# Kernel tuning notes

Hardware: AMD Instinct MI355X
Metric: run time of the kernel (lower is better)

The kernel has to match this reference:

```python
import jax, jax.numpy as jnp
import numpy as np
from jax import lax

B, C_IN, T = 32, 80, 1000
C = 512          # encoder_embedding_dim
H = C // 2       # LSTM hidden per direction
K = 5            # kernel size
P_ZONEOUT = 0.1
BN_EPS = 1e-5


def setup_inputs() -> dict:
    key = jax.random.key(0)
    ks = jax.random.split(key, 32)
    d = {"x": jax.random.normal(ks[0], (B, C_IN, T), jnp.float32)}
    in_chs = [C_IN, C, C]
    i = 1
    for l in range(3):
        cin = in_chs[l]
        d[f"cw{l}"] = jax.random.normal(ks[i], (C, cin, K), jnp.float32) * (1.0 / np.sqrt(cin * K)); i += 1
        d[f"cb{l}"] = jnp.zeros((C,), jnp.float32)
        d[f"bg{l}"] = jnp.ones((C,), jnp.float32)
        d[f"bb{l}"] = jnp.zeros((C,), jnp.float32)
        d[f"bm{l}"] = jax.random.normal(ks[i], (C,), jnp.float32) * 0.1; i += 1
        d[f"bv{l}"] = jax.random.uniform(ks[i], (C,), jnp.float32, 0.5, 1.5); i += 1
    for tag in ("f", "b"):
        d[f"wih_{tag}"] = jax.random.normal(ks[i], (4 * H, C), jnp.float32) * (1.0 / np.sqrt(C)); i += 1
        d[f"whh_{tag}"] = jax.random.normal(ks[i], (4 * H, H), jnp.float32) * (1.0 / np.sqrt(H)); i += 1
        d[f"bih_{tag}"] = jnp.zeros((4 * H,), jnp.float32)
        d[f"bhh_{tag}"] = jnp.zeros((4 * H,), jnp.float32)
    return d


def _lstm_cell(xt, h, c, wih, whh, bih, bhh):
    g = xt @ wih.T + bih + h @ whh.T + bhh          # [B, 4H]
    i, f, gg, o = jnp.split(g, 4, axis=-1)
    c2 = jax.nn.sigmoid(f) * c + jax.nn.sigmoid(i) * jnp.tanh(gg)
    h2 = jax.nn.sigmoid(o) * jnp.tanh(c2)
    return h2, c2


def _zoneout(old, new, p):
    return p * old + (1.0 - p) * new


def _encoder(x, conv_params, lstm_params):
    # conv + BN(eval) + ReLU stack; dropout is identity in eval mode
    for (cw, cb, bg, bb, bm, bv) in conv_params:
        x = lax.conv_general_dilated(x, cw, (1,), [((K - 1) // 2, (K - 1) // 2)],
                                     dimension_numbers=("NCH", "OIH", "NCH"))
        x = x + cb[None, :, None]
        x = (x - bm[None, :, None]) * (bg / jnp.sqrt(bv + BN_EPS))[None, :, None] + bb[None, :, None]
        x = jax.nn.relu(x)
    x = x.transpose(0, 2, 1)                         # [B, T, C]
    (wih_f, whh_f, bih_f, bhh_f, wih_b, whh_b, bih_b, bhh_b) = lstm_params

    xs_f = x.transpose(1, 0, 2)                      # [T, B, C] forward order
    xs_b = xs_f[::-1]                                # backward order

    def step(carry, inp):
        hf, cf, hb, cb_ = carry
        xf, xb = inp
        hf2, cf2 = _lstm_cell(xf, hf, cf, wih_f, whh_f, bih_f, bhh_f)
        hb2, cb2 = _lstm_cell(xb, hb, cb_, wih_b, whh_b, bih_b, bhh_b)
        hf = _zoneout(hf, hf2, P_ZONEOUT); cf = _zoneout(cf, cf2, P_ZONEOUT)
        hb = _zoneout(hb, hb2, P_ZONEOUT); cb_ = _zoneout(cb_, cb2, P_ZONEOUT)
        return (hf, cf, hb, cb_), (hf, hb)

    z = jnp.zeros((x.shape[0], H), x.dtype)
    _, (out_f, out_b) = lax.scan(step, (z, z, z, z), (xs_f, xs_b))
    out = jnp.concatenate([out_f, out_b[::-1]], axis=-1)  # [T, B, 2H]
    return out.transpose(1, 0, 2)                         # [B, T, 2H]


def reference(x, cw0, cb0, bg0, bb0, bm0, bv0,
              cw1, cb1, bg1, bb1, bm1, bv1,
              cw2, cb2, bg2, bb2, bm2, bv2,
              wih_f, whh_f, bih_f, bhh_f,
              wih_b, whh_b, bih_b, bhh_b):
    conv_params = [(cw0, cb0, bg0, bb0, bm0, bv0),
                   (cw1, cb1, bg1, bb1, bm1, bv1),
                   (cw2, cb2, bg2, bb2, bm2, bv2)]
    lstm_params = (wih_f, whh_f, bih_f, bhh_f, wih_b, whh_b, bih_b, bhh_b)
    return _encoder(x, conv_params, lstm_params)
```

## Files before the change

### kernel.cpp

```cpp
#include <hip/hip_runtime.h>


#define T_LEN 1000
#define NBATCH 32
#define CCH 512
#define HDIM 256
#define GDIM 1024
#define TC 100

typedef _Float16 h16;
typedef _Float16 h16x2 __attribute__((ext_vector_type(2)));
typedef _Float16 f16x8 __attribute__((ext_vector_type(8)));
typedef float    f32x4 __attribute__((ext_vector_type(4)));

__device__ __forceinline__ float fixup(float v, float alt){
    union { float f; unsigned u; } c; c.f = v;
    return ((c.u & 0x7f800000u) == 0x7f800000u) ? alt : v;
}
__device__ __forceinline__ float clamp_s(float v, float lo, float hi){
    return fminf(fmaxf(v, lo), hi);
}
__device__ __forceinline__ float sigm(float x){
    const float xc = clamp_s(x, -30.f, 30.f);
    return 1.0f / (1.0f + __expf(-xc));
}
__device__ __forceinline__ float tanh_safe(float x){
    const float ax = fminf(fabsf(x), 30.0f);
    const float t  = __expf(-2.0f * ax);
    const float r  = (1.0f - t) / (1.0f + t);
    return copysignf(r, x);
}
__device__ __forceinline__ int dot4i8(int a, int b, int c){
#if defined(__has_builtin) && __has_builtin(__builtin_amdgcn_sdot4)
    return __builtin_amdgcn_sdot4(a, b, c, false);
#else
    int r = c;
    #pragma unroll
    for (int k = 0; k < 4; ++k) {
        const int av = (a << (24 - 8*k)) >> 24;
        const int bv = (b << (24 - 8*k)) >> 24;
        r += av * bv;
    }
    return r;
#endif
}

__global__ __launch_bounds__(256)
void pack_convw_kernel(const float* __restrict__ cw, h16* __restrict__ Wp, int cin)
{
    const int n = blockIdx.x*256 + threadIdx.x;
    if (n >= 5*512*cin) return;
    const int k   = n / (512*cin);
    const int rem = n - k*512*cin;
    const int co  = rem / cin;
    const int ci  = rem - co*cin;
    Wp[n] = (h16)cw[((size_t)co*cin + ci)*5 + k];
}

__global__ __launch_bounds__(256)
void pack_wih_kernel(const float* __restrict__ wf, const float* __restrict__ wb, h16* __restrict__ Wg)
{
    const int n = blockIdx.x*256 + threadIdx.x;
    const float* src = (n < 1024*512) ? wf : wb;
    Wg[n] = (h16)src[n & (1024*512 - 1)];
}

__global__ __launch_bounds__(256)
void whh_scale_kernel(const float* __restrict__ whh_f, const float* __restrict__ whh_b,
                      float* __restrict__ scl)
{
    const int n = blockIdx.x*256 + threadIdx.x;
    if (n >= 2048) return;
    const float* whh = (n >= 1024) ? whh_b : whh_f;
    const int row = n & 1023;
    float m = 0.f;
    for (int k = 0; k < HDIM; ++k) m = fmaxf(m, fabsf(whh[(size_t)row*HDIM + k]));
    scl[n] = fmaxf(m, 1e-8f) / 16129.0f;
}

__global__ __launch_bounds__(256)
void whh_prep_kernel(const float* __restrict__ whh_f, const float* __restrict__ whh_b,
                     const float* __restrict__ scl, unsigned* __restrict__ W8)
{
    const int n = blockIdx.x * 256 + threadIdx.x;
    if (n >= 2*16*1024*4) return;
    const int dir   = n >> 16;
    const int rem   = n & 65535;
    const int chunk = rem >> 12;
    const int idx   = rem & 4095;
    const int t     = idx >> 2;
    const int e     = idx & 3;
    const float* whh = dir ? whh_b : whh_f;
    const int half = (t >> 6) & 1;
    const int qq   = t >> 7;
    const int l    = t & 63;
    const int rA   = qq*128 + 2*l;
    int row, g;
    if (chunk < 8)        { row = rA + 1; g = chunk; }
    else if (chunk < 11)  { row = rA;     g = chunk - 3; }
    else                  { row = rA;     g = chunk - 11; }
    const float inv = 1.0f / (scl[dir*1024 + row] * 127.0f);
    const int k0 = 128*half + 16*g + 4*e;
    unsigned u = 0;
    #pragma unroll
    for (int j = 0; j < 4; ++j) {
        const float w = whh[(size_t)row*HDIM + k0 + j];
        int qv = (int)rintf(w * inv);
        qv = qv > 127 ? 127 : (qv < -127 ? -127 : qv);
        u |= ((unsigned)(qv & 0xFF)) << (8*j);
    }
    W8[n] = u;
}

__global__ __launch_bounds__(256)
void x0_transpose_kernel(const float* __restrict__ x, h16* __restrict__ Xt0)
{
    const int b = blockIdx.y;
    const int t = blockIdx.x*256 + threadIdx.x;
    if (t >= T_LEN) return;
    h16 v[80];
    #pragma unroll
    for (int c = 0; c < 80; ++c) v[c] = (h16)x[((size_t)b*80 + c)*T_LEN + t];
    #pragma unroll
    for (int g = 0; g < 10; ++g)
        *(f16x8*)(Xt0 + ((size_t)b*T_LEN + t)*80 + g*8) = *(const f16x8*)(v + g*8);
}

template<int CIN>
__global__ __attribute__((amdgpu_flat_work_group_size(512,512), amdgpu_waves_per_eu(2,4)))
void conv_mfma_kernel(const h16* __restrict__ Xt, const h16* __restrict__ Wp,
                      h16* __restrict__ outp,
                      const float* __restrict__ cb, const float* __restrict__ bg,
                      const float* __restrict__ bb, const float* __restrict__ bm,
                      const float* __restrict__ bv)
{
    const int t0   = blockIdx.x * 256;
    const int co0  = blockIdx.y * 128;
    const int b    = blockIdx.z;
    const int tid  = threadIdx.x;
    const int lane = tid & 63;
    const int w    = tid >> 6;
    const int wm   = w >> 1;
    const int wn   = w & 1;
    const int lr   = lane & 15;
    const int lg   = lane >> 4;

    __shared__ __align__(16) h16 Xs[260*40];
    __shared__ __align__(16) h16 Ws[5*128*40];

    f32x4 acc[4][4];
    #pragma unroll
    for (int m = 0; m < 4; ++m)
        #pragma unroll
        for (int n = 0; n < 4; ++n)
            #pragma unroll
            for (int r = 0; r < 4; ++r) acc[m][n][r] = 0.f;

    constexpr int KSTEPS = (CIN + 31) >> 5;
    for (int cs = 0; cs < KSTEPS; ++cs) {
        const int c0 = cs << 5;
        for (int id = tid; id < 260*4; id += 512) {
            const int row = id >> 2, g = id & 3;
            const int t = t0 + row - 2;
            f16x8 v;
            #pragma unroll
            for (int j = 0; j < 8; ++j) v[j] = (h16)0.f;
            if (t >= 0 && t < T_LEN) {
                const int c = c0 + g*8;
                if (c + 8 <= CIN) {
                    v = *(const f16x8*)(Xt + ((size_t)b*T_LEN + t)*CIN + c);
                } else if (c < CIN) {
                    #pragma unroll
                    for (int j = 0; j < 8; ++j) if (c + j < CIN) v[j] = Xt[((size_t)b*T_LEN + t)*CIN + c + j];
                }
            }
            *(f16x8*)(Xs + row*40 + g*8) = v;
        }
        for (int id = tid; id < 5*128*4; id += 512) {
            const int k  = id >> 9;
            const int co = (id >> 2) & 127;
            const int g  = id & 3;
            const int c  = c0 + g*8;
            f16x8 v;
            #pragma unroll
            for (int j = 0; j < 8; ++j) v[j] = (h16)0.f;
            if (c + 8 <= CIN) {
                v = *(const f16x8*)(Wp + ((size_t)k*512 + co0 + co)*CIN + c);
            } else if (c < CIN) {
                #pragma unroll
                for (int j = 0; j < 8; ++j) if (c + j < CIN) v[j] = Wp[((size_t)k*512 + co0 + co)*CIN + c + j];
            }
            *(f16x8*)(Ws + (k*128 + co)*40 + g*8) = v;
        }
        __syncthreads();

        #pragma unroll
        for (int k = 0; k < 5; ++k) {
            f16x8 bfr[4];
            #pragma unroll
            for (int nf = 0; nf < 4; ++nf)
                bfr[nf] = *(const f16x8*)(Ws + (k*128 + wn*64 + nf*16 + lr)*40 + lg*8);
            #pragma unroll
            for (int m = 0; m < 4; ++m) {
                const f16x8 a = *(const f16x8*)(Xs + (wm*64 + m*16 + lr + k)*40 + lg*8);
                #pragma unroll
                for (int nf = 0; nf < 4; ++nf)
                    acc[m][nf] = __builtin_amdgcn_mfma_f32_16x16x32_f16(a, bfr[nf], acc[m][nf], 0, 0, 0);
            }
        }
        __syncthreads();
    }

    #pragma unroll
    for (int nf = 0; nf < 4; ++nf) {
        const int co = co0 + wn*64 + nf*16 + lr;
        const float s  = bg[co] * rsqrtf(fmaxf(bv[co] + 1e-5f, 1e-8f));
        const float sh = (cb[co] - bm[co]) * s + bb[co];
        #pragma unroll
        for (int m = 0; m < 4; ++m) {
            #pragma unroll
            for (int r = 0; r < 4; ++r) {
                const int t = t0 + wm*64 + m*16 + lg*4 + r;
                if (t < T_LEN) {
                    const float y = fixup(clamp_s(fmaxf(acc[m][nf][r]*s + sh, 0.f), 0.f, 60000.f), 0.f);
                    outp[((size_t)b*T_LEN + t)*CCH + co] = (h16)y;
                }
            }
        }
    }
}

__global__ __attribute__((amdgpu_flat_work_group_size(256,256), amdgpu_waves_per_eu(4,4)))
void gates_mfma_kernel(const h16* __restrict__ Xt,
                       const h16* __restrict__ Wg,
                       const float* __restrict__ bih_f, const float* __restrict__ bhh_f,
                       const float* __restrict__ bih_b, const float* __restrict__ bhh_b,
                       h16* __restrict__ G, int t0f, int t0b)
{
    const int tt   = blockIdx.x;
    const int r0   = blockIdx.y * 128;
    const int b    = blockIdx.z & 31;
    const int dir  = blockIdx.z >> 5;
    const int t0c  = dir ? t0b : t0f;
    const int tid  = threadIdx.x;
    const int lane = tid & 63;
    const int w    = tid >> 6;
    const int lr   = lane & 15;
    const int lg   = lane >> 4;
    const float* bi = dir ? bih_b : bih_f;
    const float* bh = dir ? bhh_b : bhh_f;
    const h16* Wd = Wg + (size_t)dir*1024*512;

    __shared__ __align__(16) h16 Xs[64*40];
    __shared__ __align__(16) h16 Ws[128*40];

    f32x4 acc[4][2];
    #pragma unroll
    for (int m = 0; m < 4; ++m)
        #pragma unroll
        for (int n = 0; n < 2; ++n)
            #pragma unroll
            for (int r = 0; r < 4; ++r) acc[m][n][r] = 0.f;

    for (int cs = 0; cs < 16; ++cs) {
        const int c0 = cs << 5;
        for (int id = tid; id < 64*4; id += 256) {
            const int row = id >> 2, g = id & 3;
            int t = t0c + tt*64 + row; if (t >= T_LEN) t = T_LEN - 1;
            *(f16x8*)(Xs + row*40 + g*8) = *(const f16x8*)(Xt + ((size_t)b*T_LEN + t)*CCH + c0 + g*8);
        }
        for (int id = tid; id < 128*4; id += 256) {
            const int row = id >> 2, g = id & 3;
            *(f16x8*)(Ws + row*40 + g*8) = *(const f16x8*)(Wd + (size_t)(r0 + row)*CCH + c0 + g*8);
        }
        __syncthreads();

        const f16x8 b0 = *(const f16x8*)(Ws + (w*32 +      lr)*40 + lg*8);
        const f16x8 b1 = *(const f16x8*)(Ws + (w*32 + 16 + lr)*40 + lg*8);
        #pragma unroll
        for (int m = 0; m < 4; ++m) {
            const f16x8 a = *(const f16x8*)(Xs + (m*16 + lr)*40 + lg*8);
            acc[m][0] = __builtin_amdgcn_mfma_f32_16x16x32_f16(a, b0, acc[m][0], 0, 0, 0);
            acc[m][1] = __builtin_amdgcn_mfma_f32_16x16x32_f16(a, b1, acc[m][1], 0, 0, 0);
        }
        __syncthreads();
    }

    #pragma unroll
    for (int nf = 0; nf < 2; ++nf) {
        const int row = r0 + w*32 + nf*16 + lr;
        const float bias = bi[row] + bh[row];
        #pragma unroll
        for (int m = 0; m < 4; ++m) {
            #pragma unroll
            for (int r = 0; r < 4; ++r) {
                const int tl = tt*64 + m*16 + lg*4 + r;
                if (tl < TC)
                    G[(((size_t)dir*TC + tl)*NBATCH + b)*GDIM + row]
                        = (h16)fixup(clamp_s(acc[m][nf][r] + bias, -60000.f, 60000.f), 0.f);
            }
        }
    }
}

__global__ __attribute__((amdgpu_flat_work_group_size(1024, 1024), amdgpu_waves_per_eu(4, 4)))
void lstm_chunk_kernel(const h16* __restrict__ G,
                       const unsigned* __restrict__ W8,
                       const float* __restrict__ scl,
                       float* __restrict__ state,
                       float* __restrict__ out,
                       int t0f, int t0b, int first)
{
    const int tid  = threadIdx.x;
    const int lane = tid & 63;
    const int half = (tid >> 6) & 1;
    const int q    = tid >> 7;
    const int dir  = blockIdx.x >> 5;
    const int b    = blockIdx.x & 31;
    const int t0   = dir ? t0b : t0f;
    float* st = state + ((size_t)(dir*NBATCH + b))*2*HDIM;
    const uint4* Wg8 = (const uint4*)W8 + (size_t)dir*16384;

    __shared__ __align__(16) uint4 lw8[5*1024];
    __shared__ __align__(4)  unsigned char hq8[256];
    __shared__ float pbuf[2*GDIM];

    uint4 rb[8];
    #pragma unroll
    for (int g = 0; g < 8; ++g) rb[g] = Wg8[g*1024 + tid];
    uint4 ra0 = Wg8[8*1024 + tid];
    uint4 ra1 = Wg8[9*1024 + tid];
    uint4 ra2 = Wg8[10*1024 + tid];

    #pragma unroll
    for (int s = 0; s < 5; ++s)
        lw8[s*1024 + tid] = Wg8[(11 + s)*1024 + tid];

    const int rA = q*128 + 2*lane;
    const float sclA = scl[dir*1024 + rA];
    const float sclB = scl[dir*1024 + rA + 1];

    float hst = 0.0f, cst = 0.0f;
    if (tid < HDIM) {
        if (!first) { hst = st[tid]; cst = st[HDIM + tid]; }
        const int qh = (int)rintf(clamp_s(hst, -1.f, 1.f) * 127.f);
        hq8[tid] = (unsigned char)(qh & 0xFF);
    }
    __syncthreads();

    float2* pbuf2 = (float2*)pbuf;
    float prev_h = 0.0f;
    int   prev_t = -1;

    for (int i = 0; i < TC; ++i) {
        const int sl = dir ? (TC - 1 - i) : i;
        const int t  = t0 + sl;
        const h16* gp = G + (((size_t)dir*TC + sl)*NBATCH + b)*GDIM;

        const unsigned wv = ((const unsigned*)hq8)[(half << 5) | (lane & 31)];

        float g0 = 0.f, g1 = 0.f, g2 = 0.f, g3 = 0.f;
        if (tid < HDIM) {
            if (prev_t >= 0)
                out[((size_t)b*T_LEN + prev_t)*(2*HDIM) + dir*HDIM + tid] = prev_h;
            g0 = (float)gp[tid];
            g1 = (float)gp[HDIM + tid];
            g2 = (float)gp[2*HDIM + tid];
            g3 = (float)gp[3*HDIM + tid];
        }

        int accA = 0, accB = 0;
        #pragma unroll
        for (int g = 0; g < 8; ++g) {
            const int s0 = __builtin_amdgcn_readlane((int)wv, 4*g + 0);
            const int s1 = __builtin_amdgcn_readlane((int)wv, 4*g + 1);
            const int s2 = __builtin_amdgcn_readlane((int)wv, 4*g + 2);
            const int s3 = __builtin_amdgcn_readlane((int)wv, 4*g + 3);
            const uint4 wA = (g < 5) ? lw8[g*1024 + tid]
                                     : (g == 5 ? ra0 : (g == 6 ? ra1 : ra2));
            const uint4 wB = rb[g];
            accA = dot4i8(s0, (int)wA.x, accA);
            accA = dot4i8(s1, (int)wA.y, accA);
            accA = dot4i8(s2, (int)wA.z, accA);
            accA = dot4i8(s3, (int)wA.w, accA);
            accB = dot4i8(s0, (int)wB.x, accB);
            accB = dot4i8(s1, (int)wB.y, accB);
            accB = dot4i8(s2, (int)wB.z, accB);
            accB = dot4i8(s3, (int)wB.w, accB);
        }

        pbuf2[(half << 9) | (q << 6) | lane] = make_float2((float)accA * sclA, (float)accB * sclB);
        __syncthreads();

        if (tid < HDIM) {
            const float gi = g0 + pbuf[tid]            + pbuf[GDIM + tid];
            const float gf = g1 + pbuf[HDIM + tid]     + pbuf[GDIM + HDIM + tid];
            const float gg = g2 + pbuf[2*HDIM + tid]   + pbuf[GDIM + 2*HDIM + tid];
            const float go = g3 + pbuf[3*HDIM + tid]   + pbuf[GDIM + 3*HDIM + tid];
            const float c2 = sigm(gf)*cst + sigm(gi)*tanh_safe(gg);
            const float h2 = sigm(go)*tanh_safe(c2);
            hst = 0.1f*hst + 0.9f*h2;
            cst = 0.1f*cst + 0.9f*c2;
            prev_h = fixup(hst, 50.0f);
            prev_t = t;
            const int qh = (int)rintf(clamp_s(hst, -1.f, 1.f) * 127.f);
            hq8[tid] = (unsigned char)(qh & 0xFF);
        }
        __syncthreads();
    }

    if (tid < HDIM) {
        if (prev_t >= 0)
            out[((size_t)b*T_LEN + prev_t)*(2*HDIM) + dir*HDIM + tid] = prev_h;
        st[tid] = hst; st[HDIM + tid] = cst;
    }
}

extern "C" void kernel_launch(void* const* d_in, const int* in_sizes, int n_in,
                              void* d_out, int out_size, void* d_ws, size_t ws_size,
                              hipStream_t stream)
{
    (void)in_sizes; (void)n_in; (void)out_size;
    if (ws_size < 49152000) return;

    const float* x     = (const float*)d_in[0];
    const float* cw0   = (const float*)d_in[1];
    const float* cb0   = (const float*)d_in[2];
    const float* bg0   = (const float*)d_in[3];
    const float* bb0   = (const float*)d_in[4];
    const float* bm0   = (const float*)d_in[5];
    const float* bv0   = (const float*)d_in[6];
    const float* cw1   = (const float*)d_in[7];
    const float* cb1   = (const float*)d_in[8];
    const float* bg1   = (const float*)d_in[9];
    const float* bb1   = (const float*)d_in[10];
    const float* bm1   = (const float*)d_in[11];
    const float* bv1   = (const float*)d_in[12];
    const float* cw2   = (const float*)d_in[13];
    const float* cb2   = (const float*)d_in[14];
    const float* bg2   = (const float*)d_in[15];
    const float* bb2   = (const float*)d_in[16];
    const float* bm2   = (const float*)d_in[17];
    const float* bv2   = (const float*)d_in[18];
    const float* wih_f = (const float*)d_in[19];
    const float* whh_f = (const float*)d_in[20];
    const float* bih_f = (const float*)d_in[21];
    const float* bhh_f = (const float*)d_in[22];
    const float* wih_b = (const float*)d_in[23];
    const float* whh_b = (const float*)d_in[24];
    const float* bih_b = (const float*)d_in[25];
    const float* bhh_b = (const float*)d_in[26];

    char* ws = (char*)d_ws;
    char* od = (char*)d_out;
    h16*      A   = (h16*)(ws);
    h16*      G   = (h16*)(ws + 32768000);
    float*    st  = (float*)(ws + 45875200);
    unsigned* W8  = (unsigned*)(ws + 46006272);
    float*    scl = (float*)(ws + 46530560);
    h16*      Wg  = (h16*)(ws + 47054848);
    h16*      Bd  = (h16*)(od);
    h16*      Wp0 = (h16*)(od + 36000000);
    h16*      Wp1 = (h16*)(od + 36409600);
    h16*      Wp2 = (h16*)(od + 41652480);
    h16*      Xt0 = (h16*)(od + 46895360);
    float*    out = (float*)d_out;

    pack_convw_kernel<<<dim3((5*512*80  + 255)/256), 256, 0, stream>>>(cw0, Wp0, 80);
    pack_convw_kernel<<<dim3((5*512*512 + 255)/256), 256, 0, stream>>>(cw1, Wp1, 512);
    pack_convw_kernel<<<dim3((5*512*512 + 255)/256), 256, 0, stream>>>(cw2, Wp2, 512);
    pack_wih_kernel<<<dim3(2*1024*512/256), 256, 0, stream>>>(wih_f, wih_b, Wg);
    whh_scale_kernel<<<dim3(8), 256, 0, stream>>>(whh_f, whh_b, scl);
    whh_prep_kernel<<<dim3(512), 256, 0, stream>>>(whh_f, whh_b, scl, W8);
    x0_transpose_kernel<<<dim3(4, 32), 256, 0, stream>>>(x, Xt0);

    const dim3 cgrid(4, 4, 32);
    conv_mfma_kernel<80> <<<cgrid, 512, 0, stream>>>(Xt0, Wp0, A,  cb0, bg0, bb0, bm0, bv0);
    conv_mfma_kernel<512><<<cgrid, 512, 0, stream>>>(A,   Wp1, Bd, cb1, bg1, bb1, bm1, bv1);
    conv_mfma_kernel<512><<<cgrid, 512, 0, stream>>>(Bd,  Wp2, A,  cb2, bg2, bb2, bm2, bv2);

    for (int c = 0; c < T_LEN / TC; ++c) {
        const int t0f = c * TC;
        const int t0b = (T_LEN - TC) - c * TC;
        gates_mfma_kernel<<<dim3(2, 8, 64), 256, 0, stream>>>(A, Wg, bih_f, bhh_f, bih_b, bhh_b, G, t0f, t0b);
        lstm_chunk_kernel<<<dim3(64), 1024, 0, stream>>>(G, W8, scl, st, out, t0f, t0b, c == 0);
    }
}
```

Baseline: 1.665 ms.

## Restructure LSTM recurrence to one thread per hidden unit with register weights

The recurrent LSTM kernel now runs 256 threads per block instead of 1024. Each thread owns one hidden unit and holds all four gate rows of int8 W_hh in 64 uint4 registers. The weight prep layout is rewritten to match, and a double-buffered hidden-state array leaves one barrier per step instead of two, removing the shared partial-sum buffer and cross-thread reduction. In exchange each thread does four times the dot-product work serially with very high register pressure (1 wave per EU), which may cause spills or lengthen the per-step critical path.

```diff
diff --git a/kernel.cpp b/kernel.cpp
--- a/kernel.cpp
+++ b/kernel.cpp
@@ -83,33 +83,28 @@
                      const float* __restrict__ scl, unsigned* __restrict__ W8)
 {
     const int n = blockIdx.x * 256 + threadIdx.x;
-    if (n >= 2*16*1024*4) return;
-    const int dir   = n >> 16;
-    const int rem   = n & 65535;
-    const int chunk = rem >> 12;
-    const int idx   = rem & 4095;
-    const int t     = idx >> 2;
-    const int e     = idx & 3;
+    if (n >= 2*64*1024) return;
+    const int dir  = n >> 16;
+    const int rem  = n & 65535;
+    const int slot = rem >> 10;
+    const int idx  = rem & 1023;
+    const int u    = idx >> 2;
+    const int e    = idx & 3;
     const float* whh = dir ? whh_b : whh_f;
-    const int half = (t >> 6) & 1;
-    const int qq   = t >> 7;
-    const int l    = t & 63;
-    const int rA   = qq*128 + 2*l;
-    int row, g;
-    if (chunk < 8)        { row = rA + 1; g = chunk; }
-    else if (chunk < 11)  { row = rA;     g = chunk - 3; }
-    else                  { row = rA;     g = chunk - 11; }
+    const int rg  = slot >> 4;
+    const int jj  = slot & 15;
+    const int row = rg*256 + u;
     const float inv = 1.0f / (scl[dir*1024 + row] * 127.0f);
-    const int k0 = 128*half + 16*g + 4*e;
-    unsigned u = 0;
+    const int k0 = 16*jj + 4*e;
+    unsigned uv = 0;
     #pragma unroll
     for (int j = 0; j < 4; ++j) {
         const float w = whh[(size_t)row*HDIM + k0 + j];
         int qv = (int)rintf(w * inv);
         qv = qv > 127 ? 127 : (qv < -127 ? -127 : qv);
-        u |= ((unsigned)(qv & 0xFF)) << (8*j);
-    }
-    W8[n] = u;
+        uv |= ((unsigned)(qv & 0xFF)) << (8*j);
+    }
+    W8[n] = uv;
 }
 
 __global__ __launch_bounds__(256)
@@ -303,7 +298,7 @@
     }
 }
 
-__global__ __attribute__((amdgpu_flat_work_group_size(1024, 1024), amdgpu_waves_per_eu(4, 4)))
+__global__ __attribute__((amdgpu_flat_work_group_size(256, 256), amdgpu_waves_per_eu(1, 1)))
 void lstm_chunk_kernel(const h16* __restrict__ G,
                        const unsigned* __restrict__ W8,
                        const float* __restrict__ scl,
@@ -311,109 +306,81 @@
                        float* __restrict__ out,
                        int t0f, int t0b, int first)
 {
-    const int tid  = threadIdx.x;
-    const int lane = tid & 63;
-    const int half = (tid >> 6) & 1;
-    const int q    = tid >> 7;
+    const int u    = threadIdx.x;
+    const int lane = u & 63;
     const int dir  = blockIdx.x >> 5;
     const int b    = blockIdx.x & 31;
     const int t0   = dir ? t0b : t0f;
     float* st = state + ((size_t)(dir*NBATCH + b))*2*HDIM;
-    const uint4* Wg8 = (const uint4*)W8 + (size_t)dir*16384;
-
-    __shared__ __align__(16) uint4 lw8[5*1024];
-    __shared__ __align__(4)  unsigned char hq8[256];
-    __shared__ float pbuf[2*GDIM];
-
-    uint4 rb[8];
-    #pragma unroll
-    for (int g = 0; g < 8; ++g) rb[g] = Wg8[g*1024 + tid];
-    uint4 ra0 = Wg8[8*1024 + tid];
-    uint4 ra1 = Wg8[9*1024 + tid];
-    uint4 ra2 = Wg8[10*1024 + tid];
-
-    #pragma unroll
-    for (int s = 0; s < 5; ++s)
-        lw8[s*1024 + tid] = Wg8[(11 + s)*1024 + tid];
-
-    const int rA = q*128 + 2*lane;
-    const float sclA = scl[dir*1024 + rA];
-    const float sclB = scl[dir*1024 + rA + 1];
+    const uint4* Wv = (const uint4*)W8 + (size_t)dir*16384;
+
+    __shared__ __align__(4) unsigned char hq8[2][256];
+
+    uint4 wr[64];
+    #pragma unroll
+    for (int s = 0; s < 64; ++s) wr[s] = Wv[s*256 + u];
+
+    const float s0 = scl[dir*1024 +       u];
+    const float s1 = scl[dir*1024 + 256 + u];
+    const float s2 = scl[dir*1024 + 512 + u];
+    const float s3 = scl[dir*1024 + 768 + u];
 
     float hst = 0.0f, cst = 0.0f;
-    if (tid < HDIM) {
-        if (!first) { hst = st[tid]; cst = st[HDIM + tid]; }
+    if (!first) { hst = st[u]; cst = st[HDIM + u]; }
+    {
         const int qh = (int)rintf(clamp_s(hst, -1.f, 1.f) * 127.f);
-        hq8[tid] = (unsigned char)(qh & 0xFF);
+        hq8[0][u] = (unsigned char)(qh & 0xFF);
     }
     __syncthreads();
-
-    float2* pbuf2 = (float2*)pbuf;
-    float prev_h = 0.0f;
-    int   prev_t = -1;
 
     for (int i = 0; i < TC; ++i) {
         const int sl = dir ? (TC - 1 - i) : i;
         const int t  = t0 + sl;
         const h16* gp = G + (((size_t)dir*TC + sl)*NBATCH + b)*GDIM;
 
-        const unsigned wv = ((const unsigned*)hq8)[(half << 5) | (lane & 31)];
-
-        float g0 = 0.f, g1 = 0.f, g2 = 0.f, g3 = 0.f;
-        if (tid < HDIM) {
-            if (prev_t >= 0)
-                out[((size_t)b*T_LEN + prev_t)*(2*HDIM) + dir*HDIM + tid] = prev_h;
-            g0 = (float)gp[tid];
-            g1 = (float)gp[HDIM + tid];
-            g2 = (float)gp[2*HDIM + tid];
-            g3 = (float)gp[3*HDIM + tid];
-        }
-
-        int accA = 0, accB = 0;
-        #pragma unroll
-        for (int g = 0; g < 8; ++g) {
-            const int s0 = __builtin_amdgcn_readlane((int)wv, 4*g + 0);
-            const int s1 = __builtin_amdgcn_readlane((int)wv, 4*g + 1);
-            const int s2 = __builtin_amdgcn_readlane((int)wv, 4*g + 2);
-            const int s3 = __builtin_amdgcn_readlane((int)wv, 4*g + 3);
-            const uint4 wA = (g < 5) ? lw8[g*1024 + tid]
-                                     : (g == 5 ? ra0 : (g == 6 ? ra1 : ra2));
-            const uint4 wB = rb[g];
-            accA = dot4i8(s0, (int)wA.x, accA);
-            accA = dot4i8(s1, (int)wA.y, accA);
-            accA = dot4i8(s2, (int)wA.z, accA);
-            accA = dot4i8(s3, (int)wA.w, accA);
-            accB = dot4i8(s0, (int)wB.x, accB);
-            accB = dot4i8(s1, (int)wB.y, accB);
-            accB = dot4i8(s2, (int)wB.z, accB);
-            accB = dot4i8(s3, (int)wB.w, accB);
-        }
-
-        pbuf2[(half << 9) | (q << 6) | lane] = make_float2((float)accA * sclA, (float)accB * sclB);
+        const float g0 = (float)gp[u];
+        const float g1 = (float)gp[256 + u];
+        const float g2 = (float)gp[512 + u];
+        const float g3 = (float)gp[768 + u];
+
+        const unsigned wv = ((const unsigned*)hq8[i & 1])[lane];
+
+        int a0 = 0, a1 = 0, a2 = 0, a3 = 0;
+        #pragma unroll
+        for (int jj = 0; jj < 16; ++jj) {
+            const int h0 = __builtin_amdgcn_readlane((int)wv, 4*jj + 0);
+            const int h1 = __builtin_amdgcn_readlane((int)wv, 4*jj + 1);
+            const int h2 = __builtin_amdgcn_readlane((int)wv, 4*jj + 2);
+            const int h3 = __builtin_amdgcn_readlane((int)wv, 4*jj + 3);
+            const uint4 w0 = wr[      jj];
+            const uint4 w1 = wr[16 + jj];
+            const uint4 w2 = wr[32 + jj];
+            const uint4 w3 = wr[48 + jj];
+            a0 = dot4i8(h0, (int)w0.x, a0); a0 = dot4i8(h1, (int)w0.y, a0);
+            a0 = dot4i8(h2, (int)w0.z, a0); a0 = dot4i8(h3, (int)w0.w, a0);
+            a1 = dot4i8(h0, (int)w1.x, a1); a1 = dot4i8(h1, (int)w1.y, a1);
+            a1 = dot4i8(h2, (int)w1.z, a1); a1 = dot4i8(h3, (int)w1.w, a1);
+            a2 = dot4i8(h0, (int)w2.x, a2); a2 = dot4i8(h1, (int)w2.y, a2);
+            a2 = dot4i8(h2, (int)w2.z, a2); a2 = dot4i8(h3, (int)w2.w, a2);
+            a3 = dot4i8(h0, (int)w3.x, a3); a3 = dot4i8(h1, (int)w3.y, a3);
+            a3 = dot4i8(h2, (int)w3.z, a3); a3 = dot4i8(h3, (int)w3.w, a3);
+        }
+
+        const float gi = g0 + (float)a0 * s0;
+        const float gf = g1 + (float)a1 * s1;
+        const float gg = g2 + (float)a2 * s2;
+        const float go = g3 + (float)a3 * s3;
+        const float c2 = sigm(gf)*cst + sigm(gi)*tanh_safe(gg);
+        const float h2v = sigm(go)*tanh_safe(c2);
+        hst = 0.1f*hst + 0.9f*h2v;
+        cst = 0.1f*cst + 0.9f*c2;
+        out[((size_t)b*T_LEN + t)*(2*HDIM) + dir*HDIM + u] = fixup(hst, 50.0f);
+        const int qh = (int)rintf(clamp_s(hst, -1.f, 1.f) * 127.f);
+        hq8[(i + 1) & 1][u] = (unsigned char)(qh & 0xFF);
         __syncthreads();
-
-        if (tid < HDIM) {
-            const float gi = g0 + pbuf[tid]            + pbuf[GDIM + tid];
-            const float gf = g1 + pbuf[HDIM + tid]     + pbuf[GDIM + HDIM + tid];
-            const float gg = g2 + pbuf[2*HDIM + tid]   + pbuf[GDIM + 2*HDIM + tid];
-            const float go = g3 + pbuf[3*HDIM + tid]   + pbuf[GDIM + 3*HDIM + tid];
-            const float c2 = sigm(gf)*cst + sigm(gi)*tanh_safe(gg);
-            const float h2 = sigm(go)*tanh_safe(c2);
-            hst = 0.1f*hst + 0.9f*h2;
-            cst = 0.1f*cst + 0.9f*c2;
-            prev_h = fixup(hst, 50.0f);
-            prev_t = t;
-            const int qh = (int)rintf(clamp_s(hst, -1.f, 1.f) * 127.f);
-            hq8[tid] = (unsigned char)(qh & 0xFF);
-        }
-        __syncthreads();
-    }
-
-    if (tid < HDIM) {
-        if (prev_t >= 0)
-            out[((size_t)b*T_LEN + prev_t)*(2*HDIM) + dir*HDIM + tid] = prev_h;
-        st[tid] = hst; st[HDIM + tid] = cst;
-    }
+    }
+
+    st[u] = hst; st[HDIM + u] = cst;
 }
 
 extern "C" void kernel_launch(void* const* d_in, const int* in_sizes, int n_in,
@@ -483,6 +450,6 @@
         const int t0f = c * TC;
         const int t0b = (T_LEN - TC) - c * TC;
         gates_mfma_kernel<<<dim3(2, 8, 64), 256, 0, stream>>>(A, Wg, bih_f, bhh_f, bih_b, bhh_b, G, t0f, t0b);
-        lstm_chunk_kernel<<<dim3(64), 1024, 0, stream>>>(G, W8, scl, st, out, t0f, t0b, c == 0);
-    }
-}
+        lstm_chunk_kernel<<<dim3(64), 256, 0, stream>>>(G, W8, scl, st, out, t0f, t0b, c == 0);
+    }
+}
```

New measurement: 1.433 ms, median of 2. 13.9% less time.
